# Performance work log

Measured on AMD Instinct MI355X. Metric: run time of the kernel, lower is better.

## Reference

```python
import jax, jax.numpy as jnp
import numpy as np

NUM_CLASSES = 22
CLIP_LENGTH = 256.0
OVERLAP_THRESH = 0.5
EPS = 1.1920929e-07  # torch.finfo(float32).eps
BOUNDS_LO = jnp.array([0., 15., 30., 60., 96., 256.], dtype=jnp.float32)
BOUNDS_HI = jnp.array([30., 60., 120., 240., 768., 768.], dtype=jnp.float32)


def setup_inputs() -> dict:
    key = jax.random.key(0)
    ks = jax.random.split(key, 9)
    B, K, C, N = 8, 100000, NUM_CLASSES, 32
    loc_data = jax.random.uniform(ks[0], (B, K, 2), jnp.float32)
    conf_data = jax.random.normal(ks[1], (B, K, C), jnp.float32)
    prop_loc_data = jax.random.uniform(ks[2], (B, K, 2), jnp.float32)
    prop_conf_data = jax.random.normal(ks[3], (B, K, C), jnp.float32)
    center_data = jax.random.normal(ks[4], (B, K, 1), jnp.float32)
    # priors: [K,2] = (center in [0,1], pyramid-level index 0..5)
    centers = (jnp.arange(K, dtype=jnp.float32) + 0.5) / K
    levels = jax.random.randint(ks[5], (K,), 0, 6).astype(jnp.float32)
    priors = jnp.stack([centers, levels], axis=-1)
    # targets: [B,N,3] = (start, end, label), label in 1..C-1
    starts = jax.random.uniform(ks[6], (B, N), jnp.float32, 0.0, 0.8)
    lens = jax.random.uniform(ks[7], (B, N), jnp.float32, 0.02, 0.3)
    ends = jnp.clip(starts + lens, 0.0, 1.0)
    labels = jax.random.randint(ks[8], (B, N), 1, C).astype(jnp.float32)
    targets = jnp.stack([starts, ends, labels], axis=-1)
    return {"loc_data": loc_data, "conf_data": conf_data,
            "prop_loc_data": prop_loc_data, "prop_conf_data": prop_conf_data,
            "center_data": center_data, "priors": priors, "targets": targets}


def _calc_iou(pred, tgt):
    # pred/tgt: [..., 2] = (left, right) distances; 1-D segment IoU
    inter = jnp.minimum(pred[..., 0], tgt[..., 0]) + jnp.minimum(pred[..., 1], tgt[..., 1])
    union = pred[..., 0] + pred[..., 1] + tgt[..., 0] + tgt[..., 1] - inter
    return inter / jnp.maximum(union, EPS)


def _giou_elem(pred, tgt):
    inter = jnp.minimum(pred[..., 0], tgt[..., 0]) + jnp.minimum(pred[..., 1], tgt[..., 1])
    union = pred[..., 0] + pred[..., 1] + tgt[..., 0] + tgt[..., 1] - inter
    ious = inter / jnp.maximum(union, EPS)
    ac = jnp.maximum(pred[..., 0], tgt[..., 0]) + jnp.maximum(pred[..., 1], tgt[..., 1])
    gious = ious - (ac - union) / jnp.maximum(ac, EPS)
    return 1.0 - gious


def _focal_sum(logits, tgt):
    # FocalLoss_Ori: softmax probs, pt = p[target]+1e-10, alpha[0]=0.25, alpha[1:]=0.75,
    # loss = -alpha_t * (1-pt)^2 * log(pt), summed over anchors -> [B]
    probs = jax.nn.softmax(logits, axis=-1)
    pt = jnp.take_along_axis(probs, tgt[..., None], axis=-1)[..., 0] + 1e-10
    alpha_t = jnp.where(tgt == 0, 0.25, 0.75)
    return (-alpha_t * (1.0 - pt) ** 2 * jnp.log(pt)).sum(axis=1)


def _forward(loc_data, conf_data, prop_loc_data, prop_conf_data, center_data, priors, targets):
    B, K, C = conf_data.shape
    maxn = 2.0 * CLIP_LENGTH

    def match():  # torch.no_grad() block
        center = priors[:, 0]                              # [K]
        lvl = priors[:, 1].astype(jnp.int32)
        lb = BOUNDS_LO[lvl][None, :, None]                 # [1,K,1]
        rb = BOUNDS_HI[lvl][None, :, None]
        ts, te = targets[..., 0], targets[..., 1]          # [B,N]
        left = (center[None, :, None] - ts[:, None, :]) * CLIP_LENGTH   # [B,K,N]
        right = (te[:, None, :] - center[None, :, None]) * CLIP_LENGTH
        max_dis = jnp.maximum(left, right)
        area = left + right
        bad = (left < 0) | (right < 0) | (max_dis <= lb) | (max_dis > rb)
        area = jnp.where(bad, maxn, area)
        best_area = area.min(axis=2)                       # [B,K]
        best_idx = area.argmin(axis=2)                     # [B,K]
        gs = jnp.take_along_axis(ts, best_idx, axis=1)
        ge = jnp.take_along_axis(te, best_idx, axis=1)
        loc_t = jnp.stack([(center[None, :] - gs) * CLIP_LENGTH,
                           (ge - center[None, :]) * CLIP_LENGTH], axis=-1)  # [B,K,2]
        labels = targets[..., 2]
        conf = jnp.take_along_axis(labels, best_idx, axis=1).astype(jnp.int32)
        conf = jnp.where(best_area >= maxn, 0, conf)
        iou = _calc_iou(loc_data, loc_t)                   # [B,K]
        pos = conf > 0
        has_pos = pos.any(axis=1)
        max_iou = jnp.where(has_pos, jnp.where(pos, iou, -jnp.inf).max(axis=1), 2.0)
        thr = jnp.minimum(OVERLAP_THRESH, max_iou)[:, None]
        prop_conf = jnp.where(iou < thr, 0, conf)
        prop_w = loc_data[..., 0] + loc_data[..., 1]
        prop_loc_t = (loc_t - loc_data) / (0.5 * prop_w[..., None])
        return loc_t, conf, prop_conf, prop_loc_t

    loc_t, conf_t, prop_conf_t, prop_loc_t = jax.lax.stop_gradient(match())
    pos = conf_t > 0                                       # [B,K]
    prop_pos = prop_conf_t > 0
    Nb = jnp.maximum(pos.sum(axis=1), 1).astype(jnp.float32)
    PNb = jnp.maximum(prop_pos.sum(axis=1), 1).astype(jnp.float32)

    # loc giou loss over positives
    loss_l = jnp.where(pos, _giou_elem(loc_data, loc_t), 0.0).sum(axis=1) / Nb

    # prop smooth_l1 over prop positives (beta=1)
    d = jnp.abs(prop_loc_data - prop_loc_t)
    sl1 = jnp.where(d < 1.0, 0.5 * d * d, d - 0.5).sum(axis=-1)   # [B,K]
    loss_prop_l = jnp.where(prop_pos, sl1, 0.0).sum(axis=1) / PNb

    # centerness BCE-with-logits vs refined IoU over positives
    prop_w = loc_data[..., 0] + loc_data[..., 1]
    cur_loc_p = 0.5 * prop_w[..., None] * prop_loc_data + loc_data
    ious_c = jnp.maximum(_calc_iou(cur_loc_p, loc_t), 0.0)
    x = center_data[..., 0]
    bce = jax.nn.softplus(x) - x * ious_c                  # BCEWithLogits(x, y)
    loss_ct = jnp.where(pos, bce, 0.0).sum(axis=1) / Nb

    # focal classification losses over ALL anchors
    loss_c = _focal_sum(conf_data, conf_t) / Nb
    loss_prop_c = _focal_sum(prop_conf_data, prop_conf_t) / PNb

    return jnp.stack([loss_l.mean(), loss_c.mean(), loss_prop_l.mean(),
                      loss_prop_c.mean(), loss_ct.mean()])


def reference(loc_data, conf_data, prop_loc_data, prop_conf_data, center_data, priors, targets):
    return _forward(loc_data, conf_data, prop_loc_data, prop_conf_data,
                    center_data, priors, targets)
```

## Files before the change

kernel.cpp:

```cpp
#include <hip/hip_runtime.h>
#include <math.h>

#define BLK 256
#define NCLS 22
#define EPSF 1.1920929e-07f
#define K1PAIRS 2
#define K1CHUNK (BLK * 2 * K1PAIRS)

__device__ __constant__ float c_lo[6] = {0.f, 15.f, 30.f, 60.f, 96.f, 256.f};
__device__ __constant__ float c_hi[6] = {30.f, 60.f, 120.f, 240.f, 768.f, 768.f};

struct MatchRes { float t0, t1; int conf; };

template <int NN>
__device__ inline MatchRes do_match_u(float center, int lvl, const float* tg) {
    float lb = c_lo[lvl], rb = c_hi[lvl];
    float best = 1e30f; int bidx = 0;
#pragma unroll
    for (int j = 0; j < NN; ++j) {
        float ts = tg[3 * j], te = tg[3 * j + 1];
        float left  = (center - ts) * 256.f;
        float right = (te - center) * 256.f;
        float md   = fmaxf(left, right);
        float area = left + right;
        bool bad = (left < 0.f) | (right < 0.f) | (md <= lb) | (md > rb);
        area = bad ? 512.f : area;
        if (area < best) { best = area; bidx = j; }
    }
    MatchRes r;
    float gs = tg[3 * bidx], ge = tg[3 * bidx + 1];
    r.t0 = (center - gs) * 256.f;
    r.t1 = (ge - center) * 256.f;
    r.conf = (best >= 512.f) ? 0 : (int)tg[3 * bidx + 2];
    return r;
}

__device__ inline MatchRes do_match_d(float center, int lvl, const float* tg, int N) {
    float lb = c_lo[lvl], rb = c_hi[lvl];
    float best = 1e30f; int bidx = 0;
    for (int j = 0; j < N; ++j) {
        float ts = tg[3 * j], te = tg[3 * j + 1];
        float left  = (center - ts) * 256.f;
        float right = (te - center) * 256.f;
        float md   = fmaxf(left, right);
        float area = left + right;
        bool bad = (left < 0.f) | (right < 0.f) | (md <= lb) | (md > rb);
        area = bad ? 512.f : area;
        if (area < best) { best = area; bidx = j; }
    }
    MatchRes r;
    float gs = tg[3 * bidx], ge = tg[3 * bidx + 1];
    r.t0 = (center - gs) * 256.f;
    r.t1 = (ge - center) * 256.f;
    r.conf = (best >= 512.f) ? 0 : (int)tg[3 * bidx + 2];
    return r;
}

__device__ inline float calc_iou(float px, float py, float t0, float t1) {
    float inter = fminf(px, t0) + fminf(py, t1);
    float uni = px + py + t0 + t1 - inter;
    return inter / fmaxf(uni, EPSF);
}

__device__ inline float vget(const float4* a, int i) {
    float4 x = a[i >> 2];
    int r = i & 3;
    return r == 0 ? x.x : (r == 1 ? x.y : (r == 2 ? x.z : x.w));
}

__device__ inline float focal22x(const float4* a, int base, int tgt) {
    float v[NCLS];
#pragma unroll
    for (int i = 0; i < NCLS; ++i) v[i] = vget(a, base + i);
    float m0 = v[0], m1 = v[1], m2 = v[2], m3 = v[3];
#pragma unroll
    for (int i = 4; i < NCLS; i += 4) {
        m0 = fmaxf(m0, v[i]);
        m1 = fmaxf(m1, v[i + 1]);
        if (i + 2 < NCLS) m2 = fmaxf(m2, v[i + 2]);
        if (i + 3 < NCLS) m3 = fmaxf(m3, v[i + 3]);
    }
    float m = fmaxf(fmaxf(m0, m1), fmaxf(m2, m3));
    float sA = 0.f, sB = 0.f, eA = 0.f, eB = 0.f;
#pragma unroll
    for (int i = 0; i < NCLS; i += 2) {
        float ea = __expf(v[i] - m);
        float eb = __expf(v[i + 1] - m);
        sA += ea; sB += eb;
        eA += (i == tgt) ? ea : 0.f;
        eB += (i + 1 == tgt) ? eb : 0.f;
    }
    float s = sA + sB;
    float pt = (eA + eB) / s + 1e-10f;
    float aa = (tgt == 0) ? 0.25f : 0.75f;
    float om = 1.f - pt;
    return -aa * om * om * __logf(pt);
}

__global__ __launch_bounds__(BLK) void k1_match(const float* __restrict__ loc,
                                                const float* __restrict__ priors,
                                                const float* __restrict__ targets,
                                                float* __restrict__ wsmax,
                                                float4* __restrict__ wsmatch,
                                                int K, int N) {
    int b = blockIdx.y;
    int chunk0 = blockIdx.x * K1CHUNK;
    __shared__ float tg[96];
    __shared__ float red[4];
    if (threadIdx.x < 3 * N) tg[threadIdx.x] = targets[b * 3 * N + threadIdx.x];
    __syncthreads();
    float my = -INFINITY;
    for (int it = 0; it < K1PAIRS; ++it) {
        int k0 = chunk0 + it * (BLK * 2) + threadIdx.x * 2;
        if (k0 < K) {
            size_t idx = (size_t)b * K + k0;
            float4 pr = reinterpret_cast<const float4*>(priors)[k0 >> 1];
            float4 lp = reinterpret_cast<const float4*>(loc)[idx >> 1];
            MatchRes r0 = (N == 32) ? do_match_u<32>(pr.x, (int)pr.y, tg)
                                    : do_match_d(pr.x, (int)pr.y, tg, N);
            MatchRes r1 = (N == 32) ? do_match_u<32>(pr.z, (int)pr.w, tg)
                                    : do_match_d(pr.z, (int)pr.w, tg, N);
            float i0 = calc_iou(lp.x, lp.y, r0.t0, r0.t1);
            float i1 = calc_iou(lp.z, lp.w, r1.t0, r1.t1);
            bool ok1 = (k0 + 1) < K;
            if (r0.conf > 0) my = fmaxf(my, i0);
            if (ok1 && r1.conf > 0) my = fmaxf(my, i1);
            if (wsmatch) {
                wsmatch[idx] = make_float4(r0.t0, r0.t1, (float)r0.conf, i0);
                if (ok1) wsmatch[idx + 1] = make_float4(r1.t0, r1.t1, (float)r1.conf, i1);
            }
        }
    }
#pragma unroll
    for (int off = 32; off; off >>= 1) my = fmaxf(my, __shfl_xor(my, off));
    int wid = threadIdx.x >> 6;
    if ((threadIdx.x & 63) == 0) red[wid] = my;
    __syncthreads();
    if (threadIdx.x == 0)
        wsmax[b * gridDim.x + blockIdx.x] =
            fmaxf(fmaxf(red[0], red[1]), fmaxf(red[2], red[3]));
}

__device__ inline void row_loss(bool act, float thr, float px, float py,
                                float plx, float ply, float xc, float4 m,
                                const float4* cr, int cbase,
                                const float4* qr, int qbase,
                                float& s_giou, float& s_sl1, float& s_bce,
                                float& s_fc, float& s_fpc,
                                float& c_pos, float& c_ppos) {
    float t0 = m.x, t1 = m.y; int cf = (int)m.z; float iou = m.w;
    int pc = (iou < thr) ? 0 : cf;
    float pw = px + py;
    if (act && cf > 0) {
        c_pos += 1.f;
        float inter = fminf(px, t0) + fminf(py, t1);
        float uni = px + py + t0 + t1 - inter;
        float ac = fmaxf(px, t0) + fmaxf(py, t1);
        float g = iou - (ac - uni) / fmaxf(ac, EPSF);
        s_giou += 1.f - g;
        float cl0 = 0.5f * pw * plx + px;
        float cl1 = 0.5f * pw * ply + py;
        float i2 = fminf(cl0, t0) + fminf(cl1, t1);
        float u2 = cl0 + cl1 + t0 + t1 - i2;
        float iouc = fmaxf(i2 / fmaxf(u2, EPSF), 0.f);
        float sp = fmaxf(xc, 0.f) + log1pf(__expf(-fabsf(xc)));
        s_bce += sp - xc * iouc;
    }
    if (act && pc > 0) {
        c_ppos += 1.f;
        float hpw = 0.5f * pw;
        float plt0 = (t0 - px) / hpw;
        float plt1 = (t1 - py) / hpw;
        float d0 = fabsf(plx - plt0), d1 = fabsf(ply - plt1);
        float f0 = (d0 < 1.f) ? 0.5f * d0 * d0 : d0 - 0.5f;
        float f1 = (d1 < 1.f) ? 0.5f * d1 * d1 : d1 - 0.5f;
        s_sl1 += f0 + f1;
    }
    if (act) {
        s_fc  += focal22x(cr, cbase, cf);
        s_fpc += focal22x(qr, qbase, pc);
    }
}

template <bool PREM>
__global__ __launch_bounds__(BLK) void k2_loss(const float* __restrict__ loc,
                                               const float* __restrict__ conf,
                                               const float* __restrict__ ploc,
                                               const float* __restrict__ pconf,
                                               const float* __restrict__ cent,
                                               const float* __restrict__ priors,
                                               const float* __restrict__ targets,
                                               const float* __restrict__ wsmax,
                                               const float4* __restrict__ wsmatch,
                                               float* __restrict__ wspart,
                                               int K, int N, int nb1) {
    int b = blockIdx.y;
    int t = blockIdx.x * BLK + threadIdx.x;
    int k0 = t * 2;
    int wid = threadIdx.x >> 6, lane = threadIdx.x & 63;
    __shared__ float tg[96];
    __shared__ float red[7][4];
    if (!PREM) {
        if (threadIdx.x < 3 * N) tg[threadIdx.x] = targets[b * 3 * N + threadIdx.x];
        __syncthreads();
    }

    float mx = -INFINITY;
    for (int j = lane; j < nb1; j += 64) mx = fmaxf(mx, wsmax[b * nb1 + j]);
#pragma unroll
    for (int off = 32; off; off >>= 1) mx = fmaxf(mx, __shfl_xor(mx, off));
    float thr = (mx == -INFINITY) ? 0.5f : fminf(0.5f, mx);

    bool a0 = k0 < K;
    int kc = a0 ? k0 : (K - 2);
    bool a1 = a0 && ((k0 + 1) < K);
    size_t idx = (size_t)b * K + kc;

    float4 c4[11], q4[11];
    {
        const float4* gc = reinterpret_cast<const float4*>(conf + idx * NCLS);
        const float4* gq = reinterpret_cast<const float4*>(pconf + idx * NCLS);
#pragma unroll
        for (int i = 0; i < 11; ++i) c4[i] = gc[i];
#pragma unroll
        for (int i = 0; i < 11; ++i) q4[i] = gq[i];
    }
    float4 lp = reinterpret_cast<const float4*>(loc)[idx >> 1];
    float4 pp = reinterpret_cast<const float4*>(ploc)[idx >> 1];
    float2 cc = reinterpret_cast<const float2*>(cent)[idx >> 1];

    float4 m0, m1;
    if (PREM) {
        m0 = wsmatch[idx];
        m1 = wsmatch[idx + 1];
    } else {
        float4 pr = reinterpret_cast<const float4*>(priors)[kc >> 1];
        MatchRes r0 = (N == 32) ? do_match_u<32>(pr.x, (int)pr.y, tg)
                                : do_match_d(pr.x, (int)pr.y, tg, N);
        MatchRes r1 = (N == 32) ? do_match_u<32>(pr.z, (int)pr.w, tg)
                                : do_match_d(pr.z, (int)pr.w, tg, N);
        m0 = make_float4(r0.t0, r0.t1, (float)r0.conf, calc_iou(lp.x, lp.y, r0.t0, r0.t1));
        m1 = make_float4(r1.t0, r1.t1, (float)r1.conf, calc_iou(lp.z, lp.w, r1.t0, r1.t1));
    }

    float s_giou = 0.f, s_sl1 = 0.f, s_bce = 0.f, s_fc = 0.f, s_fpc = 0.f,
          c_pos = 0.f, c_ppos = 0.f;
    row_loss(a0, thr, lp.x, lp.y, pp.x, pp.y, cc.x, m0, c4, 0, q4, 0,
             s_giou, s_sl1, s_bce, s_fc, s_fpc, c_pos, c_ppos);
    row_loss(a1, thr, lp.z, lp.w, pp.z, pp.w, cc.y, m1, c4, NCLS, q4, NCLS,
             s_giou, s_sl1, s_bce, s_fc, s_fpc, c_pos, c_ppos);

#pragma unroll
    for (int off = 32; off; off >>= 1) {
        s_giou += __shfl_xor(s_giou, off);
        s_sl1  += __shfl_xor(s_sl1, off);
        s_bce  += __shfl_xor(s_bce, off);
        s_fc   += __shfl_xor(s_fc, off);
        s_fpc  += __shfl_xor(s_fpc, off);
        c_pos  += __shfl_xor(c_pos, off);
        c_ppos += __shfl_xor(c_ppos, off);
    }
    if ((threadIdx.x & 63) == 0) {
        red[0][wid] = s_giou; red[1][wid] = s_sl1; red[2][wid] = s_bce;
        red[3][wid] = s_fc;   red[4][wid] = s_fpc; red[5][wid] = c_pos;
        red[6][wid] = c_ppos;
    }
    __syncthreads();
    if (threadIdx.x < 7) {
        float v = red[threadIdx.x][0] + red[threadIdx.x][1] +
                  red[threadIdx.x][2] + red[threadIdx.x][3];
        wspart[((size_t)b * gridDim.x + blockIdx.x) * 8 + threadIdx.x] = v;
    }
}

__global__ __launch_bounds__(512) void k3_final(const float* __restrict__ wspart,
                                                float* __restrict__ out, int B, int nb2) {
    int w = threadIdx.x >> 6, lane = threadIdx.x & 63;
    __shared__ float ls[8][5];
    float s[7] = {0.f, 0.f, 0.f, 0.f, 0.f, 0.f, 0.f};
    if (w < B) {
        for (int e = lane; e < nb2; e += 64) {
            const float* a = wspart + ((size_t)w * nb2 + e) * 8;
#pragma unroll
            for (int i = 0; i < 7; ++i) s[i] += a[i];
        }
    }
#pragma unroll
    for (int off = 32; off; off >>= 1)
#pragma unroll
        for (int i = 0; i < 7; ++i) s[i] += __shfl_xor(s[i], off);
    if (w < B && lane == 0) {
        float Nb  = fmaxf(s[5], 1.f);
        float PNb = fmaxf(s[6], 1.f);
        ls[w][0] = s[0] / Nb;
        ls[w][1] = s[3] / Nb;
        ls[w][2] = s[1] / PNb;
        ls[w][3] = s[4] / PNb;
        ls[w][4] = s[2] / Nb;
    }
    __syncthreads();
    if (threadIdx.x < 5) {
        float tt = 0.f;
        for (int bb = 0; bb < B; ++bb) tt += ls[bb][threadIdx.x];
        out[threadIdx.x] = tt / (float)B;
    }
}

extern "C" void kernel_launch(void* const* d_in, const int* in_sizes, int n_in,
                              void* d_out, int out_size, void* d_ws, size_t ws_size,
                              hipStream_t stream) {
    const float* loc     = (const float*)d_in[0];
    const float* conf    = (const float*)d_in[1];
    const float* ploc    = (const float*)d_in[2];
    const float* pconf   = (const float*)d_in[3];
    const float* cent    = (const float*)d_in[4];
    const float* priors  = (const float*)d_in[5];
    const float* targets = (const float*)d_in[6];
    int K = in_sizes[5] / 2;
    int B = in_sizes[0] / (2 * K);
    int N = in_sizes[6] / (3 * B);

    float* wsmax  = (float*)d_ws;
    float* wspart = (float*)d_ws + 1024;
    const size_t match_off = (size_t)1 << 20;
    float4* wsmatch = (float4*)((char*)d_ws + match_off);
    float* out = (float*)d_out;

    int nb1 = (K + K1CHUNK - 1) / K1CHUNK;
    int rows_per_blk = BLK * 2;
    int nb2 = (K + rows_per_blk - 1) / rows_per_blk;

    bool prem = (ws_size >= match_off + (size_t)B * K * 16) &&
                ((size_t)(1024 + B * nb2 * 8) * 4 <= match_off) &&
                (K % 2 == 0);

    k1_match<<<dim3(nb1, B), dim3(BLK), 0, stream>>>(loc, priors, targets, wsmax,
                                                     prem ? wsmatch : nullptr, K, N);
    if (prem)
        k2_loss<true><<<dim3(nb2, B), dim3(BLK), 0, stream>>>(
            loc, conf, ploc, pconf, cent, priors, targets, wsmax, wsmatch, wspart, K, N, nb1);
    else
        k2_loss<false><<<dim3(nb2, B), dim3(BLK), 0, stream>>>(
            loc, conf, ploc, pconf, cent, priors, targets, wsmax, wsmatch, wspart, K, N, nb1);
    k3_final<<<dim3(1), dim3(512), 0, stream>>>(wspart, out, B, nb2);
}
```

Baseline: 55.34 us.

## Recompute matching in loss kernel and stage class logits via coalesced LDS loads

The match kernel no longer writes per-anchor match records to workspace. The loss kernel recomputes the target matching itself and now maps two lanes per anchor row, one for loc and one for proposal. Confidence rows are loaded with coalesced float4 reads per wave, staged through shared memory, then read back per row for the focal loss. The match kernel is capped at a grid-stride block count. This drops a 16-byte-per-anchor write and read round trip and uncoalesced 88-byte row loads, at the cost of recomputing the 32-target match and more shared-memory traffic.

```diff
diff --git a/kernel.cpp b/kernel.cpp
--- a/kernel.cpp
+++ b/kernel.cpp
@@ -1,11 +1,16 @@
 #include <hip/hip_runtime.h>
 #include <math.h>
+#include <stdint.h>
 
 #define BLK 256
 #define NCLS 22
+#define ROWB 88
+#define WROWS 32
+#define CHB (WROWS * ROWB)
+#define CH2 (CHB / 8)
 #define EPSF 1.1920929e-07f
-#define K1PAIRS 2
-#define K1CHUNK (BLK * 2 * K1PAIRS)
+#define K1CHUNK (BLK * 4)
+#define NB1MAX 128
 
 __device__ __constant__ float c_lo[6] = {0.f, 15.f, 30.f, 60.f, 96.f, 256.f};
 __device__ __constant__ float c_hi[6] = {30.f, 60.f, 120.f, 240.f, 768.f, 768.f};
@@ -13,7 +18,7 @@
 struct MatchRes { float t0, t1; int conf; };
 
 template <int NN>
-__device__ inline MatchRes do_match_u(float center, int lvl, const float* tg) {
+__device__ __forceinline__ MatchRes do_match_u(float center, int lvl, const float* tg) {
     float lb = c_lo[lvl], rb = c_hi[lvl];
     float best = 1e30f; int bidx = 0;
 #pragma unroll
@@ -35,7 +40,7 @@
     return r;
 }
 
-__device__ inline MatchRes do_match_d(float center, int lvl, const float* tg, int N) {
+__device__ __forceinline__ MatchRes do_match_d(float center, int lvl, const float* tg, int N) {
     float lb = c_lo[lvl], rb = c_hi[lvl];
     float best = 1e30f; int bidx = 0;
     for (int j = 0; j < N; ++j) {
@@ -56,22 +61,16 @@
     return r;
 }
 
-__device__ inline float calc_iou(float px, float py, float t0, float t1) {
+__device__ __forceinline__ float calc_iou(float px, float py, float t0, float t1) {
     float inter = fminf(px, t0) + fminf(py, t1);
     float uni = px + py + t0 + t1 - inter;
     return inter / fmaxf(uni, EPSF);
 }
 
-__device__ inline float vget(const float4* a, int i) {
-    float4 x = a[i >> 2];
-    int r = i & 3;
-    return r == 0 ? x.x : (r == 1 ? x.y : (r == 2 ? x.z : x.w));
-}
-
-__device__ inline float focal22x(const float4* a, int base, int tgt) {
+__device__ __forceinline__ float focal22_lds(const float2* r2, int tgt) {
     float v[NCLS];
 #pragma unroll
-    for (int i = 0; i < NCLS; ++i) v[i] = vget(a, base + i);
+    for (int i = 0; i < NCLS / 2; ++i) { float2 x = r2[i]; v[2 * i] = x.x; v[2 * i + 1] = x.y; }
     float m0 = v[0], m1 = v[1], m2 = v[2], m3 = v[3];
 #pragma unroll
     for (int i = 4; i < NCLS; i += 4) {
@@ -90,8 +89,7 @@
         eA += (i == tgt) ? ea : 0.f;
         eB += (i + 1 == tgt) ? eb : 0.f;
     }
-    float s = sA + sB;
-    float pt = (eA + eB) / s + 1e-10f;
+    float pt = (eA + eB) / (sA + sB) + 1e-10f;
     float aa = (tgt == 0) ? 0.25f : 0.75f;
     float om = 1.f - pt;
     return -aa * om * om * __logf(pt);
@@ -101,33 +99,27 @@
                                                 const float* __restrict__ priors,
                                                 const float* __restrict__ targets,
                                                 float* __restrict__ wsmax,
-                                                float4* __restrict__ wsmatch,
                                                 int K, int N) {
     int b = blockIdx.y;
-    int chunk0 = blockIdx.x * K1CHUNK;
     __shared__ float tg[96];
     __shared__ float red[4];
     if (threadIdx.x < 3 * N) tg[threadIdx.x] = targets[b * 3 * N + threadIdx.x];
     __syncthreads();
     float my = -INFINITY;
-    for (int it = 0; it < K1PAIRS; ++it) {
-        int k0 = chunk0 + it * (BLK * 2) + threadIdx.x * 2;
-        if (k0 < K) {
-            size_t idx = (size_t)b * K + k0;
-            float4 pr = reinterpret_cast<const float4*>(priors)[k0 >> 1];
-            float4 lp = reinterpret_cast<const float4*>(loc)[idx >> 1];
-            MatchRes r0 = (N == 32) ? do_match_u<32>(pr.x, (int)pr.y, tg)
-                                    : do_match_d(pr.x, (int)pr.y, tg, N);
-            MatchRes r1 = (N == 32) ? do_match_u<32>(pr.z, (int)pr.w, tg)
-                                    : do_match_d(pr.z, (int)pr.w, tg, N);
-            float i0 = calc_iou(lp.x, lp.y, r0.t0, r0.t1);
-            float i1 = calc_iou(lp.z, lp.w, r1.t0, r1.t1);
-            bool ok1 = (k0 + 1) < K;
-            if (r0.conf > 0) my = fmaxf(my, i0);
-            if (ok1 && r1.conf > 0) my = fmaxf(my, i1);
-            if (wsmatch) {
-                wsmatch[idx] = make_float4(r0.t0, r0.t1, (float)r0.conf, i0);
-                if (ok1) wsmatch[idx + 1] = make_float4(r1.t0, r1.t1, (float)r1.conf, i1);
+    for (int base = blockIdx.x * K1CHUNK; base < K; base += gridDim.x * K1CHUNK) {
+        for (int it = 0; it < 2; ++it) {
+            int k0 = base + it * (BLK * 2) + threadIdx.x * 2;
+            if (k0 < K) {
+                size_t idx = (size_t)b * K + k0;
+                float4 pr = reinterpret_cast<const float4*>(priors)[k0 >> 1];
+                float4 lp = reinterpret_cast<const float4*>(loc)[idx >> 1];
+                MatchRes r0 = (N == 32) ? do_match_u<32>(pr.x, (int)pr.y, tg)
+                                        : do_match_d(pr.x, (int)pr.y, tg, N);
+                MatchRes r1 = (N == 32) ? do_match_u<32>(pr.z, (int)pr.w, tg)
+                                        : do_match_d(pr.z, (int)pr.w, tg, N);
+                if (r0.conf > 0) my = fmaxf(my, calc_iou(lp.x, lp.y, r0.t0, r0.t1));
+                if (((k0 + 1) < K) && r1.conf > 0)
+                    my = fmaxf(my, calc_iou(lp.z, lp.w, r1.t0, r1.t1));
             }
         }
     }
@@ -141,48 +133,7 @@
             fmaxf(fmaxf(red[0], red[1]), fmaxf(red[2], red[3]));
 }
 
-__device__ inline void row_loss(bool act, float thr, float px, float py,
-                                float plx, float ply, float xc, float4 m,
-                                const float4* cr, int cbase,
-                                const float4* qr, int qbase,
-                                float& s_giou, float& s_sl1, float& s_bce,
-                                float& s_fc, float& s_fpc,
-                                float& c_pos, float& c_ppos) {
-    float t0 = m.x, t1 = m.y; int cf = (int)m.z; float iou = m.w;
-    int pc = (iou < thr) ? 0 : cf;
-    float pw = px + py;
-    if (act && cf > 0) {
-        c_pos += 1.f;
-        float inter = fminf(px, t0) + fminf(py, t1);
-        float uni = px + py + t0 + t1 - inter;
-        float ac = fmaxf(px, t0) + fmaxf(py, t1);
-        float g = iou - (ac - uni) / fmaxf(ac, EPSF);
-        s_giou += 1.f - g;
-        float cl0 = 0.5f * pw * plx + px;
-        float cl1 = 0.5f * pw * ply + py;
-        float i2 = fminf(cl0, t0) + fminf(cl1, t1);
-        float u2 = cl0 + cl1 + t0 + t1 - i2;
-        float iouc = fmaxf(i2 / fmaxf(u2, EPSF), 0.f);
-        float sp = fmaxf(xc, 0.f) + log1pf(__expf(-fabsf(xc)));
-        s_bce += sp - xc * iouc;
-    }
-    if (act && pc > 0) {
-        c_ppos += 1.f;
-        float hpw = 0.5f * pw;
-        float plt0 = (t0 - px) / hpw;
-        float plt1 = (t1 - py) / hpw;
-        float d0 = fabsf(plx - plt0), d1 = fabsf(ply - plt1);
-        float f0 = (d0 < 1.f) ? 0.5f * d0 * d0 : d0 - 0.5f;
-        float f1 = (d1 < 1.f) ? 0.5f * d1 * d1 : d1 - 0.5f;
-        s_sl1 += f0 + f1;
-    }
-    if (act) {
-        s_fc  += focal22x(cr, cbase, cf);
-        s_fpc += focal22x(qr, qbase, pc);
-    }
-}
-
-template <bool PREM>
+template <bool UN32>
 __global__ __launch_bounds__(BLK) void k2_loss(const float* __restrict__ loc,
                                                const float* __restrict__ conf,
                                                const float* __restrict__ ploc,
@@ -191,64 +142,122 @@
                                                const float* __restrict__ priors,
                                                const float* __restrict__ targets,
                                                const float* __restrict__ wsmax,
-                                               const float4* __restrict__ wsmatch,
                                                float* __restrict__ wspart,
                                                int K, int N, int nb1) {
     int b = blockIdx.y;
-    int t = blockIdx.x * BLK + threadIdx.x;
-    int k0 = t * 2;
     int wid = threadIdx.x >> 6, lane = threadIdx.x & 63;
     __shared__ float tg[96];
     __shared__ float red[7][4];
-    if (!PREM) {
-        if (threadIdx.x < 3 * N) tg[threadIdx.x] = targets[b * 3 * N + threadIdx.x];
-        __syncthreads();
-    }
-
-    float mx = -INFINITY;
-    for (int j = lane; j < nb1; j += 64) mx = fmaxf(mx, wsmax[b * nb1 + j]);
+    __shared__ __align__(16) float2 stage[4][2 * CH2];
+    if (threadIdx.x < 3 * N) tg[threadIdx.x] = targets[b * 3 * N + threadIdx.x];
+    __syncthreads();
+
+    int rb = blockIdx.x * (4 * WROWS) + wid * WROWS;
+    int rloc = lane >> 1;
+    int r = rb + rloc;
+    bool odd = lane & 1;
+    bool act = r < K;
+    int rc = act ? r : (K - 1);
+    size_t idx = (size_t)b * K + rc;
+
+    const float* xybase = odd ? ploc : loc;
+    float2 xy = reinterpret_cast<const float2*>(xybase)[idx];
+    float ccv = cent[idx];
+    float2 pr = reinterpret_cast<const float2*>(priors)[rc];
+    float w0 = (lane < nb1) ? wsmax[b * nb1 + lane] : -INFINITY;
+    float w1 = (lane + 64 < nb1) ? wsmax[b * nb1 + lane + 64] : -INFINITY;
+
+    float4 cr[3], qr[3];
+    {
+        const uint8_t* cg = (const uint8_t*)conf;
+        const uint8_t* qg = (const uint8_t*)pconf;
+        size_t cbase = ((size_t)b * K + (size_t)(rb < K ? rb : 0)) * ROWB;
+        size_t endB = ((size_t)(b + 1) * K) * ROWB - 16;
+#pragma unroll
+        for (int i = 0; i < 3; ++i) {
+            size_t so = cbase + (size_t)i * 1024 + (size_t)lane * 16;
+            if (so > endB) so = endB;
+            cr[i] = *reinterpret_cast<const float4*>(cg + so);
+        }
+#pragma unroll
+        for (int i = 0; i < 3; ++i) {
+            size_t so = cbase + (size_t)i * 1024 + (size_t)lane * 16;
+            if (so > endB) so = endB;
+            qr[i] = *reinterpret_cast<const float4*>(qg + so);
+        }
+    }
+
+    float mx = fmaxf(w0, w1);
 #pragma unroll
     for (int off = 32; off; off >>= 1) mx = fmaxf(mx, __shfl_xor(mx, off));
     float thr = (mx == -INFINITY) ? 0.5f : fminf(0.5f, mx);
 
-    bool a0 = k0 < K;
-    int kc = a0 ? k0 : (K - 2);
-    bool a1 = a0 && ((k0 + 1) < K);
-    size_t idx = (size_t)b * K + kc;
-
-    float4 c4[11], q4[11];
+    MatchRes mr = UN32 ? do_match_u<32>(pr.x, (int)pr.y, tg)
+                       : do_match_d(pr.x, (int)pr.y, tg, N);
+    int cf = mr.conf;
+    float t0 = mr.t0, t1 = mr.t1;
+
+    float ox = __shfl_xor(xy.x, 1), oy = __shfl_xor(xy.y, 1);
+    float lpx = odd ? ox : xy.x, lpy = odd ? oy : xy.y;
+    float ppx = odd ? xy.x : ox, ppy = odd ? xy.y : oy;
+
+    float iou = calc_iou(lpx, lpy, t0, t1);
+    int pc = (iou < thr) ? 0 : cf;
+    float pw = lpx + lpy;
+
+    float s_giou = 0.f, s_sl1 = 0.f, s_bce = 0.f, c_pos = 0.f, c_ppos = 0.f;
+    if (!odd && act && cf > 0) {
+        c_pos = 1.f;
+        float inter = fminf(lpx, t0) + fminf(lpy, t1);
+        float uni = lpx + lpy + t0 + t1 - inter;
+        float ac = fmaxf(lpx, t0) + fmaxf(lpy, t1);
+        float g = iou - (ac - uni) / fmaxf(ac, EPSF);
+        s_giou = 1.f - g;
+        float cl0 = 0.5f * pw * ppx + lpx;
+        float cl1 = 0.5f * pw * ppy + lpy;
+        float i2 = fminf(cl0, t0) + fminf(cl1, t1);
+        float u2 = cl0 + cl1 + t0 + t1 - i2;
+        float iouc = fmaxf(i2 / fmaxf(u2, EPSF), 0.f);
+        float sp = fmaxf(ccv, 0.f) + log1pf(__expf(-fabsf(ccv)));
+        s_bce = sp - ccv * iouc;
+    }
+    if (odd && act && pc > 0) {
+        c_ppos = 1.f;
+        float hpw = 0.5f * pw;
+        float plt0 = (t0 - lpx) / hpw;
+        float plt1 = (t1 - lpy) / hpw;
+        float d0 = fabsf(ppx - plt0), d1 = fabsf(ppy - plt1);
+        float f0 = (d0 < 1.f) ? 0.5f * d0 * d0 : d0 - 0.5f;
+        float f1 = (d1 < 1.f) ? 0.5f * d1 * d1 : d1 - 0.5f;
+        s_sl1 = f0 + f1;
+    }
+
     {
-        const float4* gc = reinterpret_cast<const float4*>(conf + idx * NCLS);
-        const float4* gq = reinterpret_cast<const float4*>(pconf + idx * NCLS);
-#pragma unroll
-        for (int i = 0; i < 11; ++i) c4[i] = gc[i];
-#pragma unroll
-        for (int i = 0; i < 11; ++i) q4[i] = gq[i];
-    }
-    float4 lp = reinterpret_cast<const float4*>(loc)[idx >> 1];
-    float4 pp = reinterpret_cast<const float4*>(ploc)[idx >> 1];
-    float2 cc = reinterpret_cast<const float2*>(cent)[idx >> 1];
-
-    float4 m0, m1;
-    if (PREM) {
-        m0 = wsmatch[idx];
-        m1 = wsmatch[idx + 1];
-    } else {
-        float4 pr = reinterpret_cast<const float4*>(priors)[kc >> 1];
-        MatchRes r0 = (N == 32) ? do_match_u<32>(pr.x, (int)pr.y, tg)
-                                : do_match_d(pr.x, (int)pr.y, tg, N);
-        MatchRes r1 = (N == 32) ? do_match_u<32>(pr.z, (int)pr.w, tg)
-                                : do_match_d(pr.z, (int)pr.w, tg, N);
-        m0 = make_float4(r0.t0, r0.t1, (float)r0.conf, calc_iou(lp.x, lp.y, r0.t0, r0.t1));
-        m1 = make_float4(r1.t0, r1.t1, (float)r1.conf, calc_iou(lp.z, lp.w, r1.t0, r1.t1));
-    }
-
-    float s_giou = 0.f, s_sl1 = 0.f, s_bce = 0.f, s_fc = 0.f, s_fpc = 0.f,
-          c_pos = 0.f, c_ppos = 0.f;
-    row_loss(a0, thr, lp.x, lp.y, pp.x, pp.y, cc.x, m0, c4, 0, q4, 0,
-             s_giou, s_sl1, s_bce, s_fc, s_fpc, c_pos, c_ppos);
-    row_loss(a1, thr, lp.z, lp.w, pp.z, pp.w, cc.y, m1, c4, NCLS, q4, NCLS,
-             s_giou, s_sl1, s_bce, s_fc, s_fpc, c_pos, c_ppos);
+        float2* sb = stage[wid];
+#pragma unroll
+        for (int i = 0; i < 3; ++i) {
+            int e2 = i * 128 + lane * 2;
+            if (e2 < CH2) {
+                sb[e2]     = make_float2(cr[i].x, cr[i].y);
+                sb[e2 + 1] = make_float2(cr[i].z, cr[i].w);
+            }
+        }
+#pragma unroll
+        for (int i = 0; i < 3; ++i) {
+            int e2 = i * 128 + lane * 2;
+            if (e2 < CH2) {
+                sb[CH2 + e2]     = make_float2(qr[i].x, qr[i].y);
+                sb[CH2 + e2 + 1] = make_float2(qr[i].z, qr[i].w);
+            }
+        }
+    }
+    asm volatile("s_waitcnt lgkmcnt(0)" ::: "memory");
+
+    const float2* rowp = stage[wid] + (odd ? CH2 : 0) + rloc * (ROWB / 8);
+    int ftgt = odd ? pc : cf;
+    float f = act ? focal22_lds(rowp, ftgt) : 0.f;
+    float s_fc  = odd ? 0.f : f;
+    float s_fpc = odd ? f : 0.f;
 
 #pragma unroll
     for (int off = 32; off; off >>= 1) {
@@ -322,25 +331,19 @@
 
     float* wsmax  = (float*)d_ws;
     float* wspart = (float*)d_ws + 1024;
-    const size_t match_off = (size_t)1 << 20;
-    float4* wsmatch = (float4*)((char*)d_ws + match_off);
     float* out = (float*)d_out;
 
     int nb1 = (K + K1CHUNK - 1) / K1CHUNK;
-    int rows_per_blk = BLK * 2;
+    if (nb1 > NB1MAX) nb1 = NB1MAX;
+    int rows_per_blk = 4 * WROWS;
     int nb2 = (K + rows_per_blk - 1) / rows_per_blk;
 
-    bool prem = (ws_size >= match_off + (size_t)B * K * 16) &&
-                ((size_t)(1024 + B * nb2 * 8) * 4 <= match_off) &&
-                (K % 2 == 0);
-
-    k1_match<<<dim3(nb1, B), dim3(BLK), 0, stream>>>(loc, priors, targets, wsmax,
-                                                     prem ? wsmatch : nullptr, K, N);
-    if (prem)
+    k1_match<<<dim3(nb1, B), dim3(BLK), 0, stream>>>(loc, priors, targets, wsmax, K, N);
+    if (N == 32)
         k2_loss<true><<<dim3(nb2, B), dim3(BLK), 0, stream>>>(
-            loc, conf, ploc, pconf, cent, priors, targets, wsmax, wsmatch, wspart, K, N, nb1);
+            loc, conf, ploc, pconf, cent, priors, targets, wsmax, wspart, K, N, nb1);
     else
         k2_loss<false><<<dim3(nb2, B), dim3(BLK), 0, stream>>>(
-            loc, conf, ploc, pconf, cent, priors, targets, wsmax, wsmatch, wspart, K, N, nb1);
+            loc, conf, ploc, pconf, cent, priors, targets, wsmax, wspart, K, N, nb1);
     k3_final<<<dim3(1), dim3(512), 0, stream>>>(wspart, out, B, nb2);
 }
```

Result: slower. 66.99 us (+21.1%).
